# Optimization experiments

Measured on AMD Instinct MI355X. Metric: run time of the kernel, lower is better.

The kernel has to match this reference:

```python
import jax, jax.numpy as jnp
import numpy as np

N_HEADS, HEAD_D, N_LVL, N_PTS, EMB = 8, 32, 1, 4, 256


def _grid_sample(img, grid):
    """Bilinear grid_sample, align_corners=False, zeros padding.
    img: [N,C,H,W], grid: [N,Hg,Wg,2] in [-1,1] (x=width, y=height)."""
    N, C, H, W = img.shape
    x = (grid[..., 0] + 1.0) * (W * 0.5) - 0.5
    y = (grid[..., 1] + 1.0) * (H * 0.5) - 0.5
    x0 = jnp.floor(x); y0 = jnp.floor(y)
    x1 = x0 + 1.0; y1 = y0 + 1.0
    wx1 = x - x0; wx0 = 1.0 - wx1
    wy1 = y - y0; wy0 = 1.0 - wy1
    img_flat = img.reshape(N, C, H * W)

    def gather(xi, yi, w):
        xii = xi.astype(jnp.int32); yii = yi.astype(jnp.int32)
        valid = (xii >= 0) & (xii < W) & (yii >= 0) & (yii < H)
        lin = jnp.clip(yii, 0, H - 1) * W + jnp.clip(xii, 0, W - 1)   # [N,Hg,Wg]
        vals = jnp.take_along_axis(img_flat, lin.reshape(N, 1, -1), axis=2)
        vals = vals.reshape(N, C, lin.shape[1], lin.shape[2])
        return vals * (w * valid)[:, None]

    return (gather(x0, y0, wx0 * wy0) + gather(x1, y0, wx1 * wy0)
            + gather(x0, y1, wx0 * wy1) + gather(x1, y1, wx1 * wy1))


def setup_inputs() -> dict:
    key = jax.random.key(0)
    ks = jax.random.split(key, 16)
    bs, nq, Hl, Wl = 4, 10000, 100, 100
    nv = Hl * Wl
    s = 0.02
    return {
        "query": jax.random.normal(ks[0], (bs, nq, EMB), jnp.float32),
        "key": jax.random.normal(ks[1], (bs, nv, EMB), jnp.float32),
        "value": jax.random.normal(ks[2], (bs, nv, EMB), jnp.float32),
        "reference_points": jax.random.uniform(ks[3], (bs, nq, N_LVL, 2), jnp.float32),
        "Wq": s * jax.random.normal(ks[4], (HEAD_D, HEAD_D), jnp.float32),
        "bq": jnp.zeros((HEAD_D,), jnp.float32),
        "Wk": s * jax.random.normal(ks[5], (HEAD_D, HEAD_D), jnp.float32),
        "bk": jnp.zeros((HEAD_D,), jnp.float32),
        "Wv": s * jax.random.normal(ks[6], (HEAD_D, HEAD_D), jnp.float32),
        "bv": jnp.zeros((HEAD_D,), jnp.float32),
        "Woff": s * jax.random.normal(ks[7], (N_LVL * N_PTS * 2, HEAD_D), jnp.float32),
        "boff": jnp.zeros((N_LVL * N_PTS * 2,), jnp.float32),
        "Wo": s * jax.random.normal(ks[8], (EMB, EMB), jnp.float32),
        "bo": jnp.zeros((EMB,), jnp.float32),
        "spatial_shapes": jnp.array([[Hl, Wl]], dtype=jnp.int32),
    }


def reference(query, key, value, reference_points, Wq, bq, Wk, bk, Wv, bv,
              Woff, boff, Wo, bo, spatial_shapes):
    nH, D, nL, nP = N_HEADS, HEAD_D, N_LVL, N_PTS
    bs, nq, _ = query.shape
    ss = np.asarray(spatial_shapes)                      # static [L,2] (H,W)
    residual = query
    qh = query.reshape(bs, nq, nH, D)
    kh = key.reshape(bs, -1, nH, D)
    vh = value.reshape(bs, -1, nH, D)
    norm = jnp.asarray(np.stack([ss[:, 1], ss[:, 0]], -1), jnp.float32)  # (W,H) per level
    off = (qh @ Woff.T + boff).reshape(bs, nq, nH, nL, nP, 2)
    loc = reference_points[:, :, None, :, None, :] + off / norm[None, None, None, :, None, :]
    grids = 2.0 * loc - 1.0                              # [b,q,h,L,P,2]
    k_parts, v_parts = [], []
    start = 0
    for l in range(nL):
        Hl, Wl = int(ss[l, 0]), int(ss[l, 1])
        sl = slice(start, start + Hl * Wl); start += Hl * Wl
        k_img = kh[:, sl].reshape(bs, Hl * Wl, nH * D).transpose(0, 2, 1).reshape(bs * nH, D, Hl, Wl)
        v_img = vh[:, sl].reshape(bs, Hl * Wl, nH * D).transpose(0, 2, 1).reshape(bs * nH, D, Hl, Wl)
        # NOTE: key grid uses only the FIRST query's sampling locations (as in source: grids[:, :1])
        gk = grids[:, :1, :, l].transpose(0, 2, 1, 3, 4).reshape(bs * nH, 1, nP, 2)
        gv = grids[:, :, :, l].transpose(0, 2, 1, 3, 4).reshape(bs * nH, nq, nP, 2)
        k_parts.append(_grid_sample(k_img, gk))          # [bH, D, 1, P]
        v_parts.append(_grid_sample(v_img, gv))          # [bH, D, nq, P]
    k_samp = jnp.stack(k_parts, axis=-2).reshape(bs * nH, D, nL * nP)
    k_samp = k_samp.reshape(bs, nH, D, nL * nP).transpose(0, 3, 1, 2)     # [b, LP, h, d]
    v_samp = jnp.stack(v_parts, axis=-2).reshape(bs * nH, D, nq, nL * nP)  # [bH, d, q, LP]
    q = qh @ Wq.T + bq                                                    # [b, q, h, d]
    k = k_samp @ Wk.T + bk                                                # [b, LP, h, d]
    v = (v_samp.transpose(0, 2, 3, 1) @ Wv.T + bv).transpose(0, 3, 1, 2)  # [bH, d, q, LP]
    attn = jax.nn.softmax(jnp.einsum('bqhd,bkhd->bqhk', q, k), axis=-1)   # [b, q, h, LP]
    attn = attn.transpose(0, 2, 1, 3).reshape(bs * nH, 1, nq, nL * nP)
    out = (v * attn).sum(-1).reshape(bs, nH * D, nq).transpose(0, 2, 1)   # [b, q, E]
    return out @ Wo.T + bo + residual  # dropout is identity in eval mode
```

## Files before the change

kernel.cpp:

```cpp
#include <hip/hip_runtime.h>
#include <hip/hip_bf16.h>
#include <math.h>

#define NH   8
#define HD   32
#define NP   4
#define EMB  256
#define IMG_H 100
#define IMG_W 100
#define NQ   10000
#define NV   10000
#define BS   4

#define W4S 36

#define FENCE() asm volatile("" ::: "memory")

typedef __attribute__((ext_vector_type(8))) short bf16x8;
typedef __attribute__((ext_vector_type(4))) float f32x4;

#define KT_OFF    0
#define KB_OFF    16384
#define BO2_OFF   17408
#define WCF_OFF   18432
#define WCB_OFF   (18432 + 262144)
#define PREB_OFF  (18432 + 262144 + 131072)
#define WS_MIN    ((size_t)PREB_OFF)
#define WS_FULL   ((size_t)PREB_OFF + (size_t)BS * NQ * EMB * 2)

__global__ __launch_bounds__(64) void k1_keys(
    const float* __restrict__ query, const float* __restrict__ key,
    const float* __restrict__ refp,  const float* __restrict__ Woff,
    const float* __restrict__ boff,  const float* __restrict__ Wk,
    const float* __restrict__ bk,    const float* __restrict__ Wq,
    const float* __restrict__ bq,
    float* __restrict__ kt, float* __restrict__ kb)
{
    int b = blockIdx.x >> 3, h = blockIdx.x & 7;
    __shared__ float q0[HD];
    __shared__ float off[8];
    __shared__ float ks[NP][HD];
    __shared__ float kkl[NP][HD];
    int l = threadIdx.x;

    if (l < HD) q0[l] = query[(size_t)(b * NQ) * EMB + h * HD + l];
    __syncthreads();

    if (l < 8) {
        float s = boff[l];
        #pragma unroll
        for (int d = 0; d < HD; ++d) s += q0[d] * Woff[l * HD + d];
        off[l] = s;
    }
    __syncthreads();

    if (l < HD) {
        float refx = refp[(size_t)(b * NQ) * 2 + 0];
        float refy = refp[(size_t)(b * NQ) * 2 + 1];
        for (int p = 0; p < NP; ++p) {
            float x = refx * IMG_W + off[p * 2 + 0] - 0.5f;
            float y = refy * IMG_H + off[p * 2 + 1] - 0.5f;
            float x0f = floorf(x), y0f = floorf(y);
            int ix0 = (int)x0f, iy0 = (int)y0f;
            float fx = x - x0f, fy = y - y0f;
            float acc = 0.f;
            #pragma unroll
            for (int cy = 0; cy < 2; ++cy)
                #pragma unroll
                for (int cx = 0; cx < 2; ++cx) {
                    int xi = ix0 + cx, yi = iy0 + cy;
                    if ((unsigned)xi < IMG_W && (unsigned)yi < IMG_H) {
                        float wgt = (cx ? fx : 1.f - fx) * (cy ? fy : 1.f - fy);
                        acc += wgt * key[((size_t)b * NV + yi * IMG_W + xi) * EMB + h * HD + l];
                    }
                }
            ks[p][l] = acc;
        }
    }
    __syncthreads();

    #pragma unroll
    for (int t = 0; t < 2; ++t) {
        int idx = l + 64 * t;
        int p = idx >> 5, dout = idx & 31;
        float s = bk[dout];
        #pragma unroll
        for (int d = 0; d < HD; ++d) s += Wk[dout * HD + d] * ks[p][d];
        kkl[p][dout] = s;
    }
    __syncthreads();

    #pragma unroll
    for (int t = 0; t < 2; ++t) {
        int idx = l + 64 * t;
        int p = idx >> 5, d = idx & 31;
        float s = 0.f;
        #pragma unroll
        for (int dd = 0; dd < HD; ++dd) s += Wq[dd * HD + d] * kkl[p][dd];
        kt[((b * NP + p) * NH + h) * HD + d] = s;
    }
    if (l < NP) {
        float s = 0.f;
        #pragma unroll
        for (int dd = 0; dd < HD; ++dd) s += bq[dd] * kkl[l][dd];
        kb[(b * NP + l) * NH + h] = s;
    }
}

__global__ __launch_bounds__(256) void kcomb(
    const float* __restrict__ Wo, const float* __restrict__ Wv,
    const float* __restrict__ bv, const float* __restrict__ bo,
    float* __restrict__ wcf, __hip_bfloat16* __restrict__ wcb,
    float* __restrict__ bo2)
{
    __shared__ float sWv[HD * HD];
    __shared__ float sWoR[EMB];
    __shared__ float sws[4];
    int e = blockIdx.x, col = threadIdx.x;
    *(float4*)&sWv[col * 4] = *(const float4*)(Wv + col * 4);
    sWoR[col] = Wo[(size_t)e * EMB + col];
    __syncthreads();

    int h = col >> 5, d = col & 31;
    float s = 0.f;
    #pragma unroll
    for (int dd = 0; dd < HD; ++dd) s += sWoR[h * HD + dd] * sWv[dd * HD + d];
    wcf[(size_t)e * EMB + col] = s;
    wcb[(size_t)e * EMB + col] = __float2bfloat16(s);

    float pb = bv[d] * sWoR[col];
    #pragma unroll
    for (int o = 1; o < 64; o <<= 1) pb += __shfl_xor(pb, o);
    if ((col & 63) == 0) sws[col >> 6] = pb;
    __syncthreads();
    if (col == 0) bo2[e] = bo[e] + sws[0] + sws[1] + sws[2] + sws[3];
}

template<int BF16OUT>
__global__ __launch_bounds__(256) void k2_main(
    const float* __restrict__ query, const float* __restrict__ value,
    const float* __restrict__ refp,
    const float* __restrict__ Woff, const float* __restrict__ boff,
    const float* __restrict__ kt, const float* __restrict__ kb,
    float* __restrict__ pre, __hip_bfloat16* __restrict__ preb)
{
    __shared__ float sWoff[8 * W4S];
    __shared__ float sboff[8];
    __shared__ float skt[NP * NH * W4S];
    __shared__ float skb[NP * NH];
    __shared__ float qld[4][NH * W4S];
    __shared__ float offs[4][64];
    __shared__ float attnw[4][32];
    __shared__ int   soff4[4][32][4];
    __shared__ float swgt4[4][32][4];

    int tid = threadIdx.x;
    int b0 = (blockIdx.x * 4) / NQ;

    for (int i = tid; i < 8 * HD; i += 256) sWoff[(i >> 5) * W4S + (i & 31)] = Woff[i];
    if (tid < 8)  sboff[tid] = boff[tid];
    {
        int j = tid * 4;
        *(float4*)&skt[(j >> 5) * W4S + (j & 31)] =
            *(const float4*)(kt + b0 * (NP * NH * HD) + j);
    }
    if (tid < NP * NH) skb[tid] = kb[b0 * (NP * NH) + tid];

    int w = tid >> 6, lane = tid & 63;
    int gq = blockIdx.x * 4 + w;
    int b = b0;

    float4 qv = *(const float4*)(query + (size_t)gq * EMB + lane * 4);
    { int e = lane * 4; *(float4*)&qld[w][(e >> 5) * W4S + (e & 31)] = qv; }
    float refx = refp[(size_t)gq * 2 + 0];
    float refy = refp[(size_t)gq * 2 + 1];
    __syncthreads();

    int h = lane >> 3, t = lane & 7;

    float qr[HD];
    #pragma unroll
    for (int d = 0; d < HD; d += 4) {
        float4 v4 = *(const float4*)&qld[w][h * W4S + d];
        qr[d] = v4.x; qr[d + 1] = v4.y; qr[d + 2] = v4.z; qr[d + 3] = v4.w;
    }

    {
        float s = sboff[t];
        const float* wr = &sWoff[t * W4S];
        #pragma unroll
        for (int d = 0; d < HD; d += 4) {
            float4 ww = *(const float4*)(wr + d);
            s += qr[d] * ww.x + qr[d+1] * ww.y + qr[d+2] * ww.z + qr[d+3] * ww.w;
        }
        offs[w][h * 8 + t] = s;
    }

    float plog[NP];
    #pragma unroll
    for (int p = 0; p < NP; ++p) {
        const float* kr = &skt[(p * NH + h) * W4S];
        float s = 0.f;
        #pragma unroll
        for (int k = 0; k < 4; ++k) s += qr[t + 8 * k] * kr[t + 8 * k];
        plog[p] = s;
    }
    #pragma unroll
    for (int p = 0; p < NP; ++p) {
        plog[p] += __shfl_xor(plog[p], 1, 8);
        plog[p] += __shfl_xor(plog[p], 2, 8);
        plog[p] += __shfl_xor(plog[p], 4, 8);
        plog[p] += skb[p * NH + h];
    }
    {
        float mm = fmaxf(fmaxf(plog[0], plog[1]), fmaxf(plog[2], plog[3]));
        float e0 = __expf(plog[0] - mm), e1 = __expf(plog[1] - mm);
        float e2 = __expf(plog[2] - mm), e3 = __expf(plog[3] - mm);
        float inv = 1.f / (e0 + e1 + e2 + e3);
        if (t < 4) {
            float a = (t == 0) ? e0 : (t == 1) ? e1 : (t == 2) ? e2 : e3;
            attnw[w][h * 4 + t] = a * inv;
        }
    }
    FENCE();

    if (lane < 32) {
        int h2 = lane >> 2, p = lane & 3;
        float x = refx * IMG_W + offs[w][h2 * 8 + p * 2 + 0] - 0.5f;
        float y = refy * IMG_H + offs[w][h2 * 8 + p * 2 + 1] - 0.5f;
        float x0f = floorf(x), y0f = floorf(y);
        int ix0 = (int)x0f, iy0 = (int)y0f;
        float fx = x - x0f, fy = y - y0f;
        float aw = attnw[w][lane];
        float wx1 = fx * aw, wx0 = aw - wx1;
        int bbase = b * (NV * EMB) + h2 * HD;
        int   o4[4]; float g4[4];
        #pragma unroll
        for (int c = 0; c < 4; ++c) {
            int cx = c & 1, cy = c >> 1;
            int xi = ix0 + cx, yi = iy0 + cy;
            bool valid = ((unsigned)xi < IMG_W) & ((unsigned)yi < IMG_H);
            int xc = min(max(xi, 0), IMG_W - 1);
            int yc = min(max(yi, 0), IMG_H - 1);
            o4[c] = bbase + (yc * IMG_W + xc) * EMB;
            float wv = (cx ? wx1 : wx0) * (cy ? fy : 1.f - fy);
            g4[c] = valid ? wv : 0.f;
        }
        int4   ov = {o4[0], o4[1], o4[2], o4[3]};
        float4 gv = {g4[0], g4[1], g4[2], g4[3]};
        *(int4*)&soff4[w][lane][0]   = ov;
        *(float4*)&swgt4[w][lane][0] = gv;
    }
    FENCE();

    {
        int half = lane >> 5, dcol = lane & 31;
        #pragma unroll
        for (int i = 0; i < 4; ++i) {
            int hh = i * 2 + half;
            float vals[16], wv[16];
            #pragma unroll
            for (int p = 0; p < NP; ++p) {
                int hp = hh * 4 + p;
                int4   o4 = *(const int4*)&soff4[w][hp][0];
                float4 g4 = *(const float4*)&swgt4[w][hp][0];
                vals[p*4+0] = value[(unsigned)(o4.x + dcol)];
                vals[p*4+1] = value[(unsigned)(o4.y + dcol)];
                vals[p*4+2] = value[(unsigned)(o4.z + dcol)];
                vals[p*4+3] = value[(unsigned)(o4.w + dcol)];
                wv[p*4+0] = g4.x; wv[p*4+1] = g4.y; wv[p*4+2] = g4.z; wv[p*4+3] = g4.w;
            }
            float acc = 0.f;
            #pragma unroll
            for (int u = 0; u < 16; ++u) acc += wv[u] * vals[u];
            if (BF16OUT)
                preb[(size_t)gq * EMB + hh * HD + dcol] = __float2bfloat16(acc);
            else
                pre[(size_t)gq * EMB + hh * HD + dcol] = acc;
        }
    }
}

__global__ __launch_bounds__(256) void k3_mfma(
    const __hip_bfloat16* __restrict__ preb, const __hip_bfloat16* __restrict__ wcb,
    float* __restrict__ outp, const float* __restrict__ query,
    const float* __restrict__ bo2)
{
    int w = threadIdx.x >> 6, lane = threadIdx.x & 63;
    size_t m0 = (size_t)blockIdx.x * 64;
    int n0 = w * 64;
    int lr = lane & 15, lg = lane >> 4;

    const short* pa = (const short*)preb;
    const short* pb = (const short*)wcb;

    f32x4 acc[4][4];
    #pragma unroll
    for (int mt = 0; mt < 4; ++mt)
        #pragma unroll
        for (int nt = 0; nt < 4; ++nt) acc[mt][nt] = (f32x4){0.f, 0.f, 0.f, 0.f};

    #pragma unroll
    for (int k0 = 0; k0 < EMB; k0 += 32) {
        bf16x8 af[4], bf[4];
        #pragma unroll
        for (int mt = 0; mt < 4; ++mt)
            af[mt] = *(const bf16x8*)(pa + (m0 + mt * 16 + lr) * EMB + k0 + lg * 8);
        #pragma unroll
        for (int nt = 0; nt < 4; ++nt)
            bf[nt] = *(const bf16x8*)(pb + (size_t)(n0 + nt * 16 + lr) * EMB + k0 + lg * 8);
        #pragma unroll
        for (int mt = 0; mt < 4; ++mt)
            #pragma unroll
            for (int nt = 0; nt < 4; ++nt)
                acc[mt][nt] = __builtin_amdgcn_mfma_f32_16x16x32_bf16(
                    af[mt], bf[nt], acc[mt][nt], 0, 0, 0);
    }

    float bov[4];
    #pragma unroll
    for (int nt = 0; nt < 4; ++nt) bov[nt] = bo2[n0 + nt * 16 + lr];

    #pragma unroll
    for (int mt = 0; mt < 4; ++mt)
        #pragma unroll
        for (int q = 0; q < 4; ++q) {
            size_t row = m0 + mt * 16 + lg * 4 + q;
            const float* qrow = query + row * EMB;
            float* orow = outp + row * EMB;
            #pragma unroll
            for (int nt = 0; nt < 4; ++nt) {
                int col = n0 + nt * 16 + lr;
                orow[col] = acc[mt][nt][q] + bov[nt] + qrow[col];
            }
        }
}

__global__ __launch_bounds__(256) void k3_gemm(
    const float* __restrict__ pre, float* __restrict__ outp,
    const float* __restrict__ query, const float* __restrict__ wcf,
    const float* __restrict__ bo2)
{
    __shared__ float As[64 * EMB];
    int tid = threadIdx.x;
    size_t r0 = (size_t)blockIdx.x * 64;
    {
        const float4* src = (const float4*)(pre + r0 * EMB);
        float4* dst = (float4*)As;
        for (int i = tid; i < 64 * EMB / 4; i += 256) dst[i] = src[i];
    }
    __syncthreads();

    int w = tid >> 6, lane = tid & 63;
    int rb = w * 16;
    float acc[16][4];
    #pragma unroll
    for (int r = 0; r < 16; ++r)
        #pragma unroll
        for (int j = 0; j < 4; ++j) acc[r][j] = 0.f;

    for (int kc = 0; kc < EMB / 4; ++kc) {
        float4 wreg[4];
        #pragma unroll
        for (int j = 0; j < 4; ++j)
            wreg[j] = *(const float4*)&wcf[(size_t)(lane + 64 * j) * EMB + kc * 4];
        #pragma unroll
        for (int r = 0; r < 16; ++r) {
            float4 a = *(const float4*)&As[(rb + r) * EMB + kc * 4];
            #pragma unroll
            for (int j = 0; j < 4; ++j)
                acc[r][j] += a.x * wreg[j].x + a.y * wreg[j].y
                           + a.z * wreg[j].z + a.w * wreg[j].w;
        }
    }

    #pragma unroll
    for (int r = 0; r < 16; ++r) {
        size_t row = r0 + rb + r;
        #pragma unroll
        for (int j = 0; j < 4; ++j) {
            int c = lane + 64 * j;
            outp[row * EMB + c] = acc[r][j] + bo2[c] + query[row * EMB + c];
        }
    }
}

extern "C" void kernel_launch(void* const* d_in, const int* in_sizes, int n_in,
                              void* d_out, int out_size, void* d_ws, size_t ws_size,
                              hipStream_t stream) {
    const float* query = (const float*)d_in[0];
    const float* key   = (const float*)d_in[1];
    const float* value = (const float*)d_in[2];
    const float* refp  = (const float*)d_in[3];
    const float* Wq   = (const float*)d_in[4];
    const float* bq   = (const float*)d_in[5];
    const float* Wk   = (const float*)d_in[6];
    const float* bk   = (const float*)d_in[7];
    const float* Wv   = (const float*)d_in[8];
    const float* bv   = (const float*)d_in[9];
    const float* Woff = (const float*)d_in[10];
    const float* boff = (const float*)d_in[11];
    const float* Wo   = (const float*)d_in[12];
    const float* bo   = (const float*)d_in[13];
    (void)in_sizes; (void)n_in; (void)out_size;

    float* out = (float*)d_out;
    char*  ws  = (char*)d_ws;
    float* kt  = (float*)(ws + KT_OFF);
    float* kb  = (float*)(ws + KB_OFF);
    float* bo2 = (float*)(ws + BO2_OFF);
    float* wcf = (float*)(ws + WCF_OFF);
    __hip_bfloat16* wcb = (__hip_bfloat16*)(ws + WCB_OFF);

    k1_keys<<<BS * NH, 64, 0, stream>>>(query, key, refp, Woff, boff, Wk, bk,
                                        Wq, bq, kt, kb);
    kcomb<<<EMB, 256, 0, stream>>>(Wo, Wv, bv, bo, wcf, wcb, bo2);

    if (ws_size >= WS_FULL) {
        __hip_bfloat16* preb = (__hip_bfloat16*)(ws + PREB_OFF);
        k2_main<1><<<BS * NQ / 4, 256, 0, stream>>>(query, value, refp, Woff, boff,
                                                    kt, kb, nullptr, preb);
        k3_mfma<<<BS * NQ / 64, 256, 0, stream>>>(preb, wcb, out, query, bo2);
    } else {
        k2_main<0><<<BS * NQ / 4, 256, 0, stream>>>(query, value, refp, Woff, boff,
                                                    kt, kb, out, nullptr);
        k3_gemm<<<BS * NQ / 64, 256, 0, stream>>>(out, out, query, wcf, bo2);
    }
}
```

Baseline: 93.53 us.

## Merge prep kernels, drop LDS staging, vectorize value gathers as float4

Fuses the key-prep and weight-combine kernels into one launch to cut a kernel launch. In the main sampling kernel, removes shared-memory staging of query, Woff, kt and kb. Lanes now read these directly from global memory and pass offsets and attention weights between lanes with shuffles, which removes a __syncthreads. The value gather is reorganized so each lane loads float4 chunks (8 lanes per head) instead of scalar loads over 4 iterations, and writes packed bf16x4. This reduces the number of load instructions, at the cost of more redundant global/L2 reads of the small weight tensors.

```diff
diff --git a/kernel.cpp b/kernel.cpp
--- a/kernel.cpp
+++ b/kernel.cpp
@@ -12,8 +12,6 @@
 #define NV   10000
 #define BS   4
 
-#define W4S 36
-
 #define FENCE() asm volatile("" ::: "memory")
 
 typedef __attribute__((ext_vector_type(8))) short bf16x8;
@@ -25,181 +23,153 @@
 #define WCF_OFF   18432
 #define WCB_OFF   (18432 + 262144)
 #define PREB_OFF  (18432 + 262144 + 131072)
-#define WS_MIN    ((size_t)PREB_OFF)
 #define WS_FULL   ((size_t)PREB_OFF + (size_t)BS * NQ * EMB * 2)
 
-__global__ __launch_bounds__(64) void k1_keys(
+__global__ __launch_bounds__(256) void kprep(
     const float* __restrict__ query, const float* __restrict__ key,
     const float* __restrict__ refp,  const float* __restrict__ Woff,
     const float* __restrict__ boff,  const float* __restrict__ Wk,
     const float* __restrict__ bk,    const float* __restrict__ Wq,
     const float* __restrict__ bq,
-    float* __restrict__ kt, float* __restrict__ kb)
-{
-    int b = blockIdx.x >> 3, h = blockIdx.x & 7;
-    __shared__ float q0[HD];
-    __shared__ float off[8];
-    __shared__ float ks[NP][HD];
-    __shared__ float kkl[NP][HD];
-    int l = threadIdx.x;
-
-    if (l < HD) q0[l] = query[(size_t)(b * NQ) * EMB + h * HD + l];
-    __syncthreads();
-
-    if (l < 8) {
-        float s = boff[l];
-        #pragma unroll
-        for (int d = 0; d < HD; ++d) s += q0[d] * Woff[l * HD + d];
-        off[l] = s;
-    }
-    __syncthreads();
-
-    if (l < HD) {
-        float refx = refp[(size_t)(b * NQ) * 2 + 0];
-        float refy = refp[(size_t)(b * NQ) * 2 + 1];
-        for (int p = 0; p < NP; ++p) {
-            float x = refx * IMG_W + off[p * 2 + 0] - 0.5f;
-            float y = refy * IMG_H + off[p * 2 + 1] - 0.5f;
-            float x0f = floorf(x), y0f = floorf(y);
-            int ix0 = (int)x0f, iy0 = (int)y0f;
-            float fx = x - x0f, fy = y - y0f;
-            float acc = 0.f;
-            #pragma unroll
-            for (int cy = 0; cy < 2; ++cy)
-                #pragma unroll
-                for (int cx = 0; cx < 2; ++cx) {
-                    int xi = ix0 + cx, yi = iy0 + cy;
-                    if ((unsigned)xi < IMG_W && (unsigned)yi < IMG_H) {
-                        float wgt = (cx ? fx : 1.f - fx) * (cy ? fy : 1.f - fy);
-                        acc += wgt * key[((size_t)b * NV + yi * IMG_W + xi) * EMB + h * HD + l];
-                    }
-                }
-            ks[p][l] = acc;
-        }
-    }
-    __syncthreads();
-
-    #pragma unroll
-    for (int t = 0; t < 2; ++t) {
-        int idx = l + 64 * t;
-        int p = idx >> 5, dout = idx & 31;
-        float s = bk[dout];
-        #pragma unroll
-        for (int d = 0; d < HD; ++d) s += Wk[dout * HD + d] * ks[p][d];
-        kkl[p][dout] = s;
-    }
-    __syncthreads();
-
-    #pragma unroll
-    for (int t = 0; t < 2; ++t) {
-        int idx = l + 64 * t;
-        int p = idx >> 5, d = idx & 31;
-        float s = 0.f;
-        #pragma unroll
-        for (int dd = 0; dd < HD; ++dd) s += Wq[dd * HD + d] * kkl[p][dd];
-        kt[((b * NP + p) * NH + h) * HD + d] = s;
-    }
-    if (l < NP) {
-        float s = 0.f;
-        #pragma unroll
-        for (int dd = 0; dd < HD; ++dd) s += bq[dd] * kkl[l][dd];
-        kb[(b * NP + l) * NH + h] = s;
-    }
-}
-
-__global__ __launch_bounds__(256) void kcomb(
     const float* __restrict__ Wo, const float* __restrict__ Wv,
     const float* __restrict__ bv, const float* __restrict__ bo,
+    float* __restrict__ kt, float* __restrict__ kb,
     float* __restrict__ wcf, __hip_bfloat16* __restrict__ wcb,
     float* __restrict__ bo2)
 {
-    __shared__ float sWv[HD * HD];
-    __shared__ float sWoR[EMB];
-    __shared__ float sws[4];
-    int e = blockIdx.x, col = threadIdx.x;
-    *(float4*)&sWv[col * 4] = *(const float4*)(Wv + col * 4);
-    sWoR[col] = Wo[(size_t)e * EMB + col];
-    __syncthreads();
-
-    int h = col >> 5, d = col & 31;
-    float s = 0.f;
-    #pragma unroll
-    for (int dd = 0; dd < HD; ++dd) s += sWoR[h * HD + dd] * sWv[dd * HD + d];
-    wcf[(size_t)e * EMB + col] = s;
-    wcb[(size_t)e * EMB + col] = __float2bfloat16(s);
-
-    float pb = bv[d] * sWoR[col];
-    #pragma unroll
-    for (int o = 1; o < 64; o <<= 1) pb += __shfl_xor(pb, o);
-    if ((col & 63) == 0) sws[col >> 6] = pb;
-    __syncthreads();
-    if (col == 0) bo2[e] = bo[e] + sws[0] + sws[1] + sws[2] + sws[3];
+    if (blockIdx.x < EMB) {
+        __shared__ float sWv[HD * HD];
+        __shared__ float sWoR[EMB];
+        __shared__ float sws[4];
+        int e = blockIdx.x, col = threadIdx.x;
+        *(float4*)&sWv[col * 4] = *(const float4*)(Wv + col * 4);
+        sWoR[col] = Wo[(size_t)e * EMB + col];
+        __syncthreads();
+
+        int d = col & 31;
+        float s = 0.f;
+        #pragma unroll
+        for (int dd = 0; dd < HD; ++dd) s += sWoR[(col >> 5) * HD + dd] * sWv[dd * HD + d];
+        wcf[(size_t)e * EMB + col] = s;
+        if (wcb) wcb[(size_t)e * EMB + col] = __float2bfloat16(s);
+
+        float pb = bv[d] * sWoR[col];
+        #pragma unroll
+        for (int o = 1; o < 64; o <<= 1) pb += __shfl_xor(pb, o);
+        if ((col & 63) == 0) sws[col >> 6] = pb;
+        __syncthreads();
+        if (col == 0) bo2[e] = bo[e] + sws[0] + sws[1] + sws[2] + sws[3];
+    } else {
+        int bh = blockIdx.x - EMB;
+        int b = bh >> 3, h = bh & 7;
+        __shared__ float q0[HD];
+        __shared__ float off[8];
+        __shared__ float ks[NP][HD];
+        __shared__ float kkl[NP][HD];
+        int l = threadIdx.x;
+
+        if (l < HD) q0[l] = query[(size_t)(b * NQ) * EMB + h * HD + l];
+        __syncthreads();
+
+        if (l < 8) {
+            float s = boff[l];
+            #pragma unroll
+            for (int d = 0; d < HD; ++d) s += q0[d] * Woff[l * HD + d];
+            off[l] = s;
+        }
+        __syncthreads();
+
+        if (l < HD) {
+            float refx = refp[(size_t)(b * NQ) * 2 + 0];
+            float refy = refp[(size_t)(b * NQ) * 2 + 1];
+            for (int p = 0; p < NP; ++p) {
+                float x = refx * IMG_W + off[p * 2 + 0] - 0.5f;
+                float y = refy * IMG_H + off[p * 2 + 1] - 0.5f;
+                float x0f = floorf(x), y0f = floorf(y);
+                int ix0 = (int)x0f, iy0 = (int)y0f;
+                float fx = x - x0f, fy = y - y0f;
+                float acc = 0.f;
+                #pragma unroll
+                for (int cy = 0; cy < 2; ++cy)
+                    #pragma unroll
+                    for (int cx = 0; cx < 2; ++cx) {
+                        int xi = ix0 + cx, yi = iy0 + cy;
+                        if ((unsigned)xi < IMG_W && (unsigned)yi < IMG_H) {
+                            float wgt = (cx ? fx : 1.f - fx) * (cy ? fy : 1.f - fy);
+                            acc += wgt * key[((size_t)b * NV + yi * IMG_W + xi) * EMB + h * HD + l];
+                        }
+                    }
+                ks[p][l] = acc;
+            }
+        }
+        __syncthreads();
+
+        if (l < 128) {
+            int p = l >> 5, dout = l & 31;
+            float s = bk[dout];
+            #pragma unroll
+            for (int d = 0; d < HD; ++d) s += Wk[dout * HD + d] * ks[p][d];
+            kkl[p][dout] = s;
+        }
+        __syncthreads();
+
+        if (l < 128) {
+            int p = l >> 5, d = l & 31;
+            float s = 0.f;
+            #pragma unroll
+            for (int dd = 0; dd < HD; ++dd) s += Wq[dd * HD + d] * kkl[p][dd];
+            kt[((b * NP + p) * NH + h) * HD + d] = s;
+        }
+        if (l < NP) {
+            float s = 0.f;
+            #pragma unroll
+            for (int dd = 0; dd < HD; ++dd) s += bq[dd] * kkl[l][dd];
+            kb[(b * NP + l) * NH + h] = s;
+        }
+    }
 }
 
 template<int BF16OUT>
-__global__ __launch_bounds__(256) void k2_main(
+__global__ __launch_bounds__(256) void k2n(
     const float* __restrict__ query, const float* __restrict__ value,
     const float* __restrict__ refp,
     const float* __restrict__ Woff, const float* __restrict__ boff,
     const float* __restrict__ kt, const float* __restrict__ kb,
     float* __restrict__ pre, __hip_bfloat16* __restrict__ preb)
 {
-    __shared__ float sWoff[8 * W4S];
-    __shared__ float sboff[8];
-    __shared__ float skt[NP * NH * W4S];
-    __shared__ float skb[NP * NH];
-    __shared__ float qld[4][NH * W4S];
-    __shared__ float offs[4][64];
-    __shared__ float attnw[4][32];
     __shared__ int   soff4[4][32][4];
     __shared__ float swgt4[4][32][4];
 
     int tid = threadIdx.x;
-    int b0 = (blockIdx.x * 4) / NQ;
-
-    for (int i = tid; i < 8 * HD; i += 256) sWoff[(i >> 5) * W4S + (i & 31)] = Woff[i];
-    if (tid < 8)  sboff[tid] = boff[tid];
-    {
-        int j = tid * 4;
-        *(float4*)&skt[(j >> 5) * W4S + (j & 31)] =
-            *(const float4*)(kt + b0 * (NP * NH * HD) + j);
-    }
-    if (tid < NP * NH) skb[tid] = kb[b0 * (NP * NH) + tid];
-
     int w = tid >> 6, lane = tid & 63;
     int gq = blockIdx.x * 4 + w;
-    int b = b0;
-
-    float4 qv = *(const float4*)(query + (size_t)gq * EMB + lane * 4);
-    { int e = lane * 4; *(float4*)&qld[w][(e >> 5) * W4S + (e & 31)] = qv; }
+    int b = (blockIdx.x * 4) / NQ;
+    int h = lane >> 3, t = lane & 7;
+
+    float qr[HD];
+    const float* qrow = query + (size_t)gq * EMB + h * HD;
+    #pragma unroll
+    for (int d = 0; d < HD; d += 4) {
+        float4 v4 = *(const float4*)(qrow + d);
+        qr[d] = v4.x; qr[d + 1] = v4.y; qr[d + 2] = v4.z; qr[d + 3] = v4.w;
+    }
     float refx = refp[(size_t)gq * 2 + 0];
     float refy = refp[(size_t)gq * 2 + 1];
-    __syncthreads();
-
-    int h = lane >> 3, t = lane & 7;
-
-    float qr[HD];
-    #pragma unroll
-    for (int d = 0; d < HD; d += 4) {
-        float4 v4 = *(const float4*)&qld[w][h * W4S + d];
-        qr[d] = v4.x; qr[d + 1] = v4.y; qr[d + 2] = v4.z; qr[d + 3] = v4.w;
-    }
-
+
+    float offv = boff[t];
     {
-        float s = sboff[t];
-        const float* wr = &sWoff[t * W4S];
+        const float* wr = Woff + t * HD;
         #pragma unroll
         for (int d = 0; d < HD; d += 4) {
             float4 ww = *(const float4*)(wr + d);
-            s += qr[d] * ww.x + qr[d+1] * ww.y + qr[d+2] * ww.z + qr[d+3] * ww.w;
-        }
-        offs[w][h * 8 + t] = s;
+            offv += qr[d]*ww.x + qr[d+1]*ww.y + qr[d+2]*ww.z + qr[d+3]*ww.w;
+        }
     }
 
     float plog[NP];
     #pragma unroll
     for (int p = 0; p < NP; ++p) {
-        const float* kr = &skt[(p * NH + h) * W4S];
+        const float* kr = kt + ((b * NP + p) * NH + h) * HD;
         float s = 0.f;
         #pragma unroll
         for (int k = 0; k < 4; ++k) s += qr[t + 8 * k] * kr[t + 8 * k];
@@ -210,73 +180,80 @@
         plog[p] += __shfl_xor(plog[p], 1, 8);
         plog[p] += __shfl_xor(plog[p], 2, 8);
         plog[p] += __shfl_xor(plog[p], 4, 8);
-        plog[p] += skb[p * NH + h];
-    }
+        plog[p] += kb[(b * NP + p) * NH + h];
+    }
+    float aval = 0.f;
     {
         float mm = fmaxf(fmaxf(plog[0], plog[1]), fmaxf(plog[2], plog[3]));
-        float e0 = __expf(plog[0] - mm), e1 = __expf(plog[1] - mm);
-        float e2 = __expf(plog[2] - mm), e3 = __expf(plog[3] - mm);
+        float e0 = __expf(plog[0]-mm), e1 = __expf(plog[1]-mm);
+        float e2 = __expf(plog[2]-mm), e3 = __expf(plog[3]-mm);
         float inv = 1.f / (e0 + e1 + e2 + e3);
-        if (t < 4) {
-            float a = (t == 0) ? e0 : (t == 1) ? e1 : (t == 2) ? e2 : e3;
-            attnw[w][h * 4 + t] = a * inv;
+        if (t < 4) aval = ((t == 0) ? e0 : (t == 1) ? e1 : (t == 2) ? e2 : e3) * inv;
+    }
+
+    {
+        int ll = lane & 31;
+        int h2 = ll >> 2, p2 = ll & 3;
+        float mox = __shfl(offv, h2 * 8 + 2 * p2);
+        float moy = __shfl(offv, h2 * 8 + 2 * p2 + 1);
+        float maw = __shfl(aval, h2 * 8 + p2);
+        if (lane < 32) {
+            float x = refx * IMG_W + mox - 0.5f;
+            float y = refy * IMG_H + moy - 0.5f;
+            float x0f = floorf(x), y0f = floorf(y);
+            int ix0 = (int)x0f, iy0 = (int)y0f;
+            float fx = x - x0f, fy = y - y0f;
+            float wx1 = fx * maw, wx0 = maw - wx1;
+            int bbase = b * (NV * EMB) + h2 * HD;
+            int   o4[4]; float g4[4];
+            #pragma unroll
+            for (int c = 0; c < 4; ++c) {
+                int cx = c & 1, cy = c >> 1;
+                int xi = ix0 + cx, yi = iy0 + cy;
+                bool valid = ((unsigned)xi < IMG_W) & ((unsigned)yi < IMG_H);
+                int xc = min(max(xi, 0), IMG_W - 1);
+                int yc = min(max(yi, 0), IMG_H - 1);
+                o4[c] = (bbase + (yc * IMG_W + xc) * EMB) * 4;
+                float wv = (cx ? wx1 : wx0) * (cy ? fy : 1.f - fy);
+                g4[c] = valid ? wv : 0.f;
+            }
+            int4   ov = {o4[0], o4[1], o4[2], o4[3]};
+            float4 gv = {g4[0], g4[1], g4[2], g4[3]};
+            *(int4*)&soff4[w][ll][0]   = ov;
+            *(float4*)&swgt4[w][ll][0] = gv;
         }
     }
     FENCE();
 
-    if (lane < 32) {
-        int h2 = lane >> 2, p = lane & 3;
-        float x = refx * IMG_W + offs[w][h2 * 8 + p * 2 + 0] - 0.5f;
-        float y = refy * IMG_H + offs[w][h2 * 8 + p * 2 + 1] - 0.5f;
-        float x0f = floorf(x), y0f = floorf(y);
-        int ix0 = (int)x0f, iy0 = (int)y0f;
-        float fx = x - x0f, fy = y - y0f;
-        float aw = attnw[w][lane];
-        float wx1 = fx * aw, wx0 = aw - wx1;
-        int bbase = b * (NV * EMB) + h2 * HD;
-        int   o4[4]; float g4[4];
-        #pragma unroll
-        for (int c = 0; c < 4; ++c) {
-            int cx = c & 1, cy = c >> 1;
-            int xi = ix0 + cx, yi = iy0 + cy;
-            bool valid = ((unsigned)xi < IMG_W) & ((unsigned)yi < IMG_H);
-            int xc = min(max(xi, 0), IMG_W - 1);
-            int yc = min(max(yi, 0), IMG_H - 1);
-            o4[c] = bbase + (yc * IMG_W + xc) * EMB;
-            float wv = (cx ? wx1 : wx0) * (cy ? fy : 1.f - fy);
-            g4[c] = valid ? wv : 0.f;
-        }
-        int4   ov = {o4[0], o4[1], o4[2], o4[3]};
-        float4 gv = {g4[0], g4[1], g4[2], g4[3]};
-        *(int4*)&soff4[w][lane][0]   = ov;
-        *(float4*)&swgt4[w][lane][0] = gv;
-    }
-    FENCE();
-
     {
-        int half = lane >> 5, dcol = lane & 31;
-        #pragma unroll
-        for (int i = 0; i < 4; ++i) {
-            int hh = i * 2 + half;
-            float vals[16], wv[16];
-            #pragma unroll
-            for (int p = 0; p < NP; ++p) {
-                int hp = hh * 4 + p;
-                int4   o4 = *(const int4*)&soff4[w][hp][0];
-                float4 g4 = *(const float4*)&swgt4[w][hp][0];
-                vals[p*4+0] = value[(unsigned)(o4.x + dcol)];
-                vals[p*4+1] = value[(unsigned)(o4.y + dcol)];
-                vals[p*4+2] = value[(unsigned)(o4.z + dcol)];
-                vals[p*4+3] = value[(unsigned)(o4.w + dcol)];
-                wv[p*4+0] = g4.x; wv[p*4+1] = g4.y; wv[p*4+2] = g4.z; wv[p*4+3] = g4.w;
-            }
-            float acc = 0.f;
-            #pragma unroll
-            for (int u = 0; u < 16; ++u) acc += wv[u] * vals[u];
-            if (BF16OUT)
-                preb[(size_t)gq * EMB + hh * HD + dcol] = __float2bfloat16(acc);
-            else
-                pre[(size_t)gq * EMB + hh * HD + dcol] = acc;
+        unsigned co = t * 16;
+        const char* vb = (const char*)value;
+        float4 acc = {0.f, 0.f, 0.f, 0.f};
+        #pragma unroll
+        for (int p = 0; p < NP; ++p) {
+            int hp = h * 4 + p;
+            int4   o4 = *(const int4*)&soff4[w][hp][0];
+            float4 g4 = *(const float4*)&swgt4[w][hp][0];
+            float4 v0 = *(const float4*)(vb + (unsigned)o4.x + co);
+            float4 v1 = *(const float4*)(vb + (unsigned)o4.y + co);
+            float4 v2 = *(const float4*)(vb + (unsigned)o4.z + co);
+            float4 v3 = *(const float4*)(vb + (unsigned)o4.w + co);
+            acc.x += g4.x*v0.x + g4.y*v1.x + g4.z*v2.x + g4.w*v3.x;
+            acc.y += g4.x*v0.y + g4.y*v1.y + g4.z*v2.y + g4.w*v3.y;
+            acc.z += g4.x*v0.z + g4.y*v1.z + g4.z*v2.z + g4.w*v3.z;
+            acc.w += g4.x*v0.w + g4.y*v1.w + g4.z*v2.w + g4.w*v3.w;
+        }
+        int cb = t * 4;
+        if (BF16OUT) {
+            __hip_bfloat16 pk[4];
+            pk[0] = __float2bfloat16(acc.x);
+            pk[1] = __float2bfloat16(acc.y);
+            pk[2] = __float2bfloat16(acc.z);
+            pk[3] = __float2bfloat16(acc.w);
+            *(ushort4*)((unsigned short*)preb + (size_t)gq * EMB + h * HD + cb) =
+                *(const ushort4*)&pk[0];
+        } else {
+            *(float4*)(pre + (size_t)gq * EMB + h * HD + cb) = acc;
         }
     }
 }
@@ -412,18 +389,20 @@
     float* wcf = (float*)(ws + WCF_OFF);
     __hip_bfloat16* wcb = (__hip_bfloat16*)(ws + WCB_OFF);
 
-    k1_keys<<<BS * NH, 64, 0, stream>>>(query, key, refp, Woff, boff, Wk, bk,
-                                        Wq, bq, kt, kb);
-    kcomb<<<EMB, 256, 0, stream>>>(Wo, Wv, bv, bo, wcf, wcb, bo2);
-
-    if (ws_size >= WS_FULL) {
+    bool full = (ws_size >= WS_FULL);
+
+    kprep<<<EMB + BS * NH, 256, 0, stream>>>(query, key, refp, Woff, boff, Wk, bk,
+                                             Wq, bq, Wo, Wv, bv, bo,
+                                             kt, kb, wcf, full ? wcb : nullptr, bo2);
+
+    if (full) {
         __hip_bfloat16* preb = (__hip_bfloat16*)(ws + PREB_OFF);
-        k2_main<1><<<BS * NQ / 4, 256, 0, stream>>>(query, value, refp, Woff, boff,
-                                                    kt, kb, nullptr, preb);
+        k2n<1><<<BS * NQ / 4, 256, 0, stream>>>(query, value, refp, Woff, boff,
+                                                kt, kb, nullptr, preb);
         k3_mfma<<<BS * NQ / 64, 256, 0, stream>>>(preb, wcb, out, query, bo2);
     } else {
-        k2_main<0><<<BS * NQ / 4, 256, 0, stream>>>(query, value, refp, Woff, boff,
-                                                    kt, kb, out, nullptr);
+        k2n<0><<<BS * NQ / 4, 256, 0, stream>>>(query, value, refp, Woff, boff,
+                                                kt, kb, out, nullptr);
         k3_gemm<<<BS * NQ / 64, 256, 0, stream>>>(out, out, query, wcf, bo2);
     }
 }
```

After: 120.8 us. 1.29x slower.
